# Kernel optimization log

Measured on AMD Instinct MI355X. Metric: run time of the kernel, lower is better.

Reference implementation:

```python
import jax, jax.numpy as jnp
import numpy as np

IN_FEATURES = 512
OUT_FEATURES = 256
N = 2048

def setup_inputs() -> dict:
    key = jax.random.key(0)
    k1, k2, k3 = jax.random.split(key, 3)
    x = jax.random.normal(k1, (N, IN_FEATURES), dtype=jnp.float32)
    # kaiming_uniform_(a=sqrt(5)) -> uniform(-b, b) with b = sqrt(6/((1+5)*fan_in)) = 1/sqrt(fan_in)
    bound_w = 1.0 / np.sqrt(IN_FEATURES)
    weight = jax.random.uniform(k2, (OUT_FEATURES, IN_FEATURES), dtype=jnp.float32,
                                minval=-bound_w, maxval=bound_w)
    bound_b = 1.0 / np.sqrt(IN_FEATURES)
    bias = jax.random.uniform(k3, (OUT_FEATURES,), dtype=jnp.float32,
                              minval=-bound_b, maxval=bound_b)
    return {"x": x, "weight": weight, "bias": bias}

def reference(x, weight, bias):
    # MAM fully-connected (beta == 0 path):
    # prod[n, k, j] = x[n, k] * weight[j, k]
    # C[n, j] = max_k prod[n,k,j] + min_k prod[n,k,j] + bias[j]
    prod = x[:, :, None] * weight.T[None, :, :]   # [N, in, out]
    C = jnp.max(prod, axis=1) + jnp.min(prod, axis=1) + bias[None, :]
    return C
```

## Files before the change

### kernel.cpp

```cpp
#include <hip/hip_runtime.h>
#include <math.h>

#define N_ 2048
#define K_ 512
#define J_ 256

typedef __attribute__((address_space(3))) float       lds_f;
typedef const __attribute__((address_space(1))) float glb_f;

#define MAX3(acc, a, b) asm("v_max3_f32 %0, %0, %1, %2" : "+v"(acc) : "v"(a), "v"(b))
#define MIN3(acc, a, b) asm("v_min3_f32 %0, %0, %1, %2" : "+v"(acc) : "v"(a), "v"(b))

__global__ __launch_bounds__(512) void mam_fused6(
    const float* __restrict__ x, const float* __restrict__ w,
    const float* __restrict__ bias, float* __restrict__ out)
{
    __shared__ __align__(16) float xls[8 * 512];
    __shared__ __align__(16) float cmb[8 * 8 * 128 * 2];

    const int t    = threadIdx.x;
    const int lane = t & 63;
    const int kc   = __builtin_amdgcn_readfirstlane(t >> 6);

    const int wg0 = (int)blockIdx.x;
    const int wg  = (wg0 & 7) * 64 + (wg0 >> 3);
    const int jg  = wg & 1;
    const int ng  = wg >> 1;

    const int n0    = ng * 8;
    const int jbase = jg * 128;

    __builtin_amdgcn_global_load_lds(
        (glb_f*)(x + (size_t)(n0 + kc) * K_ + lane * 4),
        (lds_f*)(xls + kc * 512), 16, 0, 0);
    __builtin_amdgcn_global_load_lds(
        (glb_f*)(x + (size_t)(n0 + kc) * K_ + 256 + lane * 4),
        (lds_f*)(xls + kc * 512 + 256), 16, 0, 0);

    float4 wreg[2][16];
#pragma unroll
    for (int jj = 0; jj < 2; ++jj) {
        const float4* wp =
            (const float4*)(w + (size_t)(jbase + jj * 64 + lane) * K_ + kc * 64);
#pragma unroll
        for (int g = 0; g < 16; ++g) wreg[jj][g] = wp[g];
    }

    __syncthreads();

    float mx[8][2], mn[8][2];
#pragma unroll
    for (int n = 0; n < 8; ++n)
#pragma unroll
        for (int jj = 0; jj < 2; ++jj) {
            mx[n][jj] = -__builtin_inff();
            mn[n][jj] =  __builtin_inff();
        }

#pragma unroll
    for (int n = 0; n < 8; ++n) {
#pragma unroll
        for (int gb = 0; gb < 4; ++gb) {
            float4 xv[4];
#pragma unroll
            for (int g = 0; g < 4; ++g)
                xv[g] = *(const float4*)&xls[n * 512 + kc * 64 + gb * 16 + g * 4];
#pragma unroll
            for (int g = 0; g < 4; ++g) {
#pragma unroll
                for (int jj = 0; jj < 2; ++jj) {
                    const float4 wv = wreg[jj][gb * 4 + g];
                    const float p0 = xv[g].x * wv.x;
                    const float p1 = xv[g].y * wv.y;
                    const float p2 = xv[g].z * wv.z;
                    const float p3 = xv[g].w * wv.w;
                    MAX3(mx[n][jj], p0, p1); MAX3(mx[n][jj], p2, p3);
                    MIN3(mn[n][jj], p0, p1); MIN3(mn[n][jj], p2, p3);
                }
            }
        }
    }

#pragma unroll
    for (int n = 0; n < 8; ++n)
#pragma unroll
        for (int jj = 0; jj < 2; ++jj) {
            float2 v; v.x = mx[n][jj]; v.y = mn[n][jj];
            *(float2*)&cmb[((kc * 8 + n) * 128 + jj * 64 + lane) * 2] = v;
        }
    __syncthreads();

#pragma unroll
    for (int i = 0; i < 2; ++i) {
        const int u    = t + i * 512;
        const int n    = u >> 7;
        const int jcol = u & 127;
        float a = -__builtin_inff(), b = __builtin_inff();
#pragma unroll
        for (int c = 0; c < 8; ++c) {
            const float2 p = *(const float2*)&cmb[((c * 8 + n) * 128 + jcol) * 2];
            a = fmaxf(a, p.x);
            b = fminf(b, p.y);
        }
        out[(size_t)(n0 + n) * J_ + jbase + jcol] = a + b + bias[jbase + jcol];
    }
}

extern "C" void kernel_launch(void* const* d_in, const int* in_sizes, int n_in,
                              void* d_out, int out_size, void* d_ws, size_t ws_size,
                              hipStream_t stream) {
    const float* x    = (const float*)d_in[0];
    const float* w    = (const float*)d_in[1];
    const float* bias = (const float*)d_in[2];
    float* out = (float*)d_out;

    dim3 grid(512);
    mam_fused6<<<grid, 512, 0, stream>>>(x, w, bias, out);
}
```

Measured before the change: 86.71 us.

## Switch to 32x32 output tiles with x and w staged in swizzled LDS

```diff
diff --git a/kernel.cpp b/kernel.cpp
--- a/kernel.cpp
+++ b/kernel.cpp
@@ -5,104 +5,113 @@
 #define K_ 512
 #define J_ 256
 
+typedef float f32x4 __attribute__((ext_vector_type(4)));
 typedef __attribute__((address_space(3))) float       lds_f;
 typedef const __attribute__((address_space(1))) float glb_f;
 
 #define MAX3(acc, a, b) asm("v_max3_f32 %0, %0, %1, %2" : "+v"(acc) : "v"(a), "v"(b))
 #define MIN3(acc, a, b) asm("v_min3_f32 %0, %0, %1, %2" : "+v"(acc) : "v"(a), "v"(b))
 
-__global__ __launch_bounds__(512) void mam_fused6(
+__global__ __launch_bounds__(512, 2) void mam_fused9(
     const float* __restrict__ x, const float* __restrict__ w,
     const float* __restrict__ bias, float* __restrict__ out)
 {
-    __shared__ __align__(16) float xls[8 * 512];
-    __shared__ __align__(16) float cmb[8 * 8 * 128 * 2];
+    __shared__ __align__(16) float sm[32768];
+
+    float* xs  = sm;
+    float* wsh = sm + 16384;
 
     const int t    = threadIdx.x;
     const int lane = t & 63;
-    const int kc   = __builtin_amdgcn_readfirstlane(t >> 6);
+    const int kq   = __builtin_amdgcn_readfirstlane(t >> 6);
 
     const int wg0 = (int)blockIdx.x;
     const int wg  = (wg0 & 7) * 64 + (wg0 >> 3);
-    const int jg  = wg & 1;
-    const int ng  = wg >> 1;
+    const int bx  = wg & 7;
+    const int by  = wg >> 3;
+    const int n0  = by * 32;
+    const int j0  = bx * 32;
 
-    const int n0    = ng * 8;
-    const int jbase = jg * 128;
+    const int rn = lane >> 3;
+    const int cj = lane & 7;
 
-    __builtin_amdgcn_global_load_lds(
-        (glb_f*)(x + (size_t)(n0 + kc) * K_ + lane * 4),
-        (lds_f*)(xls + kc * 512), 16, 0, 0);
-    __builtin_amdgcn_global_load_lds(
-        (glb_f*)(x + (size_t)(n0 + kc) * K_ + 256 + lane * 4),
-        (lds_f*)(xls + kc * 512 + 256), 16, 0, 0);
+#pragma unroll
+    for (int p = 0; p < 4; ++p) {
+        const int row = kq * 4 + p;
+        const int so  = (lane ^ (row & 7)) << 2;
+#pragma unroll
+        for (int h = 0; h < 2; ++h) {
+            __builtin_amdgcn_global_load_lds(
+                (glb_f*)(x + (size_t)(n0 + row) * K_ + h * 256 + so),
+                (lds_f*)(xs + row * 512 + h * 256), 16, 0, 0);
+            __builtin_amdgcn_global_load_lds(
+                (glb_f*)(w + (size_t)(j0 + row) * K_ + h * 256 + so),
+                (lds_f*)(wsh + row * 512 + h * 256), 16, 0, 0);
+        }
+    }
 
-    float4 wreg[2][16];
+    float mx[4][4], mn[4][4];
 #pragma unroll
-    for (int jj = 0; jj < 2; ++jj) {
-        const float4* wp =
-            (const float4*)(w + (size_t)(jbase + jj * 64 + lane) * K_ + kc * 64);
+    for (int i = 0; i < 4; ++i)
 #pragma unroll
-        for (int g = 0; g < 16; ++g) wreg[jj][g] = wp[g];
+        for (int jj = 0; jj < 4; ++jj) {
+            mx[i][jj] = -__builtin_inff();
+            mn[i][jj] =  __builtin_inff();
+        }
+
+    __syncthreads();
+
+    const int xb = rn * 512 + kq * 64;
+    const int wb = cj * 512 + kq * 64;
+
+#pragma unroll
+    for (int q = 0; q < 16; ++q) {
+        const int xo = xb + ((q ^ rn) << 2);
+        const int wo = wb + ((q ^ cj) << 2);
+        f32x4 xv[4], wv[4];
+#pragma unroll
+        for (int i = 0; i < 4; ++i)
+            xv[i] = *(const f32x4*)&xs[xo + i * 4096];
+#pragma unroll
+        for (int jj = 0; jj < 4; ++jj)
+            wv[jj] = *(const f32x4*)&wsh[wo + jj * 4096];
+#pragma unroll
+        for (int i = 0; i < 4; ++i)
+#pragma unroll
+            for (int jj = 0; jj < 4; ++jj) {
+                const f32x4 a = xv[i], b = wv[jj];
+                const float p0 = a.x * b.x, p1 = a.y * b.y;
+                const float p2 = a.z * b.z, p3 = a.w * b.w;
+                MAX3(mx[i][jj], p0, p1); MAX3(mx[i][jj], p2, p3);
+                MIN3(mn[i][jj], p0, p1); MIN3(mn[i][jj], p2, p3);
+            }
     }
 
     __syncthreads();
 
-    float mx[8][2], mn[8][2];
+    float2* cb = (float2*)sm;
 #pragma unroll
-    for (int n = 0; n < 8; ++n)
+    for (int i = 0; i < 4; ++i)
 #pragma unroll
-        for (int jj = 0; jj < 2; ++jj) {
-            mx[n][jj] = -__builtin_inff();
-            mn[n][jj] =  __builtin_inff();
-        }
-
-#pragma unroll
-    for (int n = 0; n < 8; ++n) {
-#pragma unroll
-        for (int gb = 0; gb < 4; ++gb) {
-            float4 xv[4];
-#pragma unroll
-            for (int g = 0; g < 4; ++g)
-                xv[g] = *(const float4*)&xls[n * 512 + kc * 64 + gb * 16 + g * 4];
-#pragma unroll
-            for (int g = 0; g < 4; ++g) {
-#pragma unroll
-                for (int jj = 0; jj < 2; ++jj) {
-                    const float4 wv = wreg[jj][gb * 4 + g];
-                    const float p0 = xv[g].x * wv.x;
-                    const float p1 = xv[g].y * wv.y;
-                    const float p2 = xv[g].z * wv.z;
-                    const float p3 = xv[g].w * wv.w;
-                    MAX3(mx[n][jj], p0, p1); MAX3(mx[n][jj], p2, p3);
-                    MIN3(mn[n][jj], p0, p1); MIN3(mn[n][jj], p2, p3);
-                }
-            }
-        }
-    }
-
-#pragma unroll
-    for (int n = 0; n < 8; ++n)
-#pragma unroll
-        for (int jj = 0; jj < 2; ++jj) {
-            float2 v; v.x = mx[n][jj]; v.y = mn[n][jj];
-            *(float2*)&cmb[((kc * 8 + n) * 128 + jj * 64 + lane) * 2] = v;
+        for (int jj = 0; jj < 4; ++jj) {
+            const int r = rn + 8 * i, c = cj + 8 * jj;
+            float2 v; v.x = mx[i][jj]; v.y = mn[i][jj];
+            cb[(kq * 32 + r) * 36 + c] = v;
         }
     __syncthreads();
 
 #pragma unroll
-    for (int i = 0; i < 2; ++i) {
-        const int u    = t + i * 512;
-        const int n    = u >> 7;
-        const int jcol = u & 127;
+    for (int e = 0; e < 2; ++e) {
+        const int o = t + e * 512;
+        const int r = o >> 5, c = o & 31;
         float a = -__builtin_inff(), b = __builtin_inff();
 #pragma unroll
-        for (int c = 0; c < 8; ++c) {
-            const float2 p = *(const float2*)&cmb[((c * 8 + n) * 128 + jcol) * 2];
-            a = fmaxf(a, p.x);
-            b = fminf(b, p.y);
+        for (int kk = 0; kk < 8; ++kk) {
+            const float2 v = cb[(kk * 32 + r) * 36 + c];
+            a = fmaxf(a, v.x);
+            b = fminf(b, v.y);
         }
-        out[(size_t)(n0 + n) * J_ + jbase + jcol] = a + b + bias[jbase + jcol];
+        out[(size_t)(n0 + r) * J_ + j0 + c] = a + b + bias[j0 + c];
     }
 }
 
@@ -115,5 +124,5 @@
     float* out = (float*)d_out;
 
     dim3 grid(512);
-    mam_fused6<<<grid, 512, 0, stream>>>(x, w, bias, out);
+    mam_fused9<<<grid, 512, 0, stream>>>(x, w, bias, out);
 }
```

After: 74.06 us. 1.17x faster.
